# Performance work log

Hardware: AMD Instinct MI355X
Metric: run time of the kernel (lower is better)

Reference implementation:

```python
import jax, jax.numpy as jnp
import numpy as np

S, B, D, H = 1024, 8, 768, 12
PROMPT_NUM = 8
DH = D // H


def setup_inputs() -> dict:
    key = jax.random.key(0)
    ks = jax.random.split(key, 5)
    scale = 1.0 / np.sqrt(D)
    return {
        "x": jax.random.normal(ks[0], (S, B, D), dtype=jnp.float32),
        "in_proj_weight": jax.random.normal(ks[1], (3 * D, D), dtype=jnp.float32) * scale,
        "in_proj_bias": jax.random.normal(ks[2], (3 * D,), dtype=jnp.float32) * 0.02,
        "out_w": jax.random.normal(ks[3], (D, D), dtype=jnp.float32) * scale,
        "out_b": jax.random.normal(ks[4], (D,), dtype=jnp.float32) * 0.02,
    }


def reference(x, in_proj_weight, in_proj_bias, out_w, out_b):
    # x: (S, B, D) -> (B, S, D)
    xt = jnp.transpose(x, (1, 0, 2))
    qkv = xt @ in_proj_weight.T + in_proj_bias  # (B, S, 3D)
    q, k, v = jnp.split(qkv, 3, axis=-1)
    q = q.reshape(B, S, H, DH)
    k = k.reshape(B, S, H, DH)
    v = v.reshape(B, S, H, DH)
    # affinity (n, q, k, h); scale by sqrt(head_dim)
    aff = jnp.einsum("nqhc,nkhc->nqkh", q / np.sqrt(DH), k)
    # prompt masking: CLS_MASK | PROMPT_MASK
    tokens = S - PROMPT_NUM
    m = np.zeros((S, S), dtype=bool)
    m[0, tokens:] = True          # CLS_MASK: CLS query can't attend to prompts
    m[tokens:, tokens:] = True    # PROMPT_MASK: prompts can't attend to prompts
    m = jnp.asarray(m)
    aff = jnp.where(m[None, :, :, None], jnp.float32(-10000.0), aff)
    # softmax over key axis (dim=-2 of nqkh)
    aff = jax.nn.softmax(aff, axis=2)
    mix = jnp.einsum("nqlh,nlhc->nqhc", aff, v)  # (B, S, H, DH)
    out = mix.reshape(B, S, D) @ out_w.T + out_b
    # transpose back to (S, B, ...)
    return (
        jnp.transpose(q, (1, 0, 2, 3)),
        jnp.transpose(k, (1, 0, 2, 3)),
        jnp.transpose(v, (1, 0, 2, 3)),
        jnp.transpose(out, (1, 0, 2)),
    )
```

## Files before the change

kernel.cpp:

```cpp
#include <hip/hip_runtime.h>


typedef unsigned short u16;
typedef __attribute__((ext_vector_type(8))) short short8;
typedef __attribute__((ext_vector_type(4))) short short4v;
typedef __attribute__((ext_vector_type(4))) float floatx4;
typedef __attribute__((ext_vector_type(4))) unsigned short ushort4v;

#define NB 8
#define NS 1024
#define NH 12
#define ND 768
#define DHD 64
#define TOKENS 1016
#define QKV_OUT_STRIDE 6291456

#if __has_builtin(__builtin_amdgcn_exp2f)
#define EXP2(x) __builtin_amdgcn_exp2f(x)
#else
#define EXP2(x) exp2f(x)
#endif

#if defined(__HIP_DEVICE_COMPILE__)
  #if __has_builtin(__builtin_amdgcn_mfma_f32_16x16x16bf16_1k)
    #define MFMA16(a, b, c) __builtin_amdgcn_mfma_f32_16x16x16bf16_1k(a, b, c, 0, 0, 0)
  #else
    #define MFMA16(a, b, c) __builtin_amdgcn_mfma_f32_16x16x16_bf16(a, b, c, 0, 0, 0)
  #endif
  #define GLD16(g, l)                                                        \
    __builtin_amdgcn_global_load_lds(                                        \
        (const __attribute__((address_space(1))) void*)(g),                  \
        (__attribute__((address_space(3))) void*)(l), 16, 0, 0)
#else
  #define MFMA16(a, b, c) (c)
  #define GLD16(g, l) ((void)0)
#endif

__device__ __forceinline__ u16 f2bf(float f) {
  union { float f; unsigned u; } c; c.f = f;
  return (u16)((c.u + 0x7fffu + ((c.u >> 16) & 1u)) >> 16);
}

#define CVT_B0 6144
#define CVT_B1 1728
#define CVT_B2 576
__global__ __launch_bounds__(256) void cvt3(
    const float* __restrict__ s0, u16* __restrict__ d0,
    const float* __restrict__ s1, u16* __restrict__ d1,
    const float* __restrict__ s2, u16* __restrict__ d2) {
  int blk = blockIdx.x;
  const float* s; u16* d;
  if (blk < CVT_B0) { s = s0; d = d0; }
  else if (blk < CVT_B0 + CVT_B1) { s = s1; d = d1; blk -= CVT_B0; }
  else { s = s2; d = d2; blk -= CVT_B0 + CVT_B1; }
  const int i = (blk * 256 + (int)threadIdx.x) * 4;
  const float4 v = *(const float4*)(s + i);
  ushort4v o;
  o.x = f2bf(v.x); o.y = f2bf(v.y); o.z = f2bf(v.z); o.w = f2bf(v.w);
  *(ushort4v*)(d + i) = o;
}

__global__ __launch_bounds__(256) void qkv_gemm(
    const u16* __restrict__ Xb, const u16* __restrict__ Wb,
    const float* __restrict__ bias, float* __restrict__ out) {
  __shared__ __align__(16) u16 As[128][32];
  __shared__ __align__(16) u16 Bs[128][32];
  const int tid = threadIdx.x;
  const int lane = tid & 63, wave = tid >> 6;
  const int l15 = lane & 15, quad = lane >> 4;
  const int wm = wave & 1, wn = wave >> 1;
  const int mblk = blockIdx.x * 128;
  const int nblk = blockIdx.y * 128;

  floatx4 acc[4][4];
#pragma unroll
  for (int i = 0; i < 4; ++i)
#pragma unroll
    for (int j = 0; j < 4; ++j) acc[i][j] = (floatx4)0.f;

  const int lr = lane >> 2;
  const int lc = (lane & 3) * 8;
  const int c0 = wave * 2;
  const int r0 = c0 * 16 + lr, r1 = r0 + 16;
  const int gm0 = mblk + r0, gm1 = mblk + r1;
  const u16* ga0 = Xb + ((gm0 & 1023) * NB + (gm0 >> 10)) * ND + lc;
  const u16* ga1 = Xb + ((gm1 & 1023) * NB + (gm1 >> 10)) * ND + lc;
  const u16* gb0 = Wb + (nblk + r0) * ND + lc;
  const u16* gb1 = Wb + (nblk + r1) * ND + lc;
  u16* la0 = &As[c0 * 16][0];
  u16* la1 = &As[c0 * 16 + 16][0];
  u16* lb0 = &Bs[c0 * 16][0];
  u16* lb1 = &Bs[c0 * 16 + 16][0];

  for (int kt = 0; kt < 24; ++kt) {
    const int k0 = kt * 32;
    GLD16(ga0 + k0, la0);
    GLD16(ga1 + k0, la1);
    GLD16(gb0 + k0, lb0);
    GLD16(gb1 + k0, lb1);
    __syncthreads();
    short8 af[4], bfr[4];
#pragma unroll
    for (int mt = 0; mt < 4; ++mt)
      af[mt] = *(const short8*)&As[wm * 64 + mt * 16 + l15][quad * 8];
#pragma unroll
    for (int nt = 0; nt < 4; ++nt)
      bfr[nt] = *(const short8*)&Bs[wn * 64 + nt * 16 + l15][quad * 8];
#pragma unroll
    for (int mt = 0; mt < 4; ++mt)
#pragma unroll
      for (int nt = 0; nt < 4; ++nt)
        acc[mt][nt] = __builtin_amdgcn_mfma_f32_16x16x32_bf16(
            af[mt], bfr[nt], acc[mt][nt], 0, 0, 0);
    __syncthreads();
  }

#pragma unroll
  for (int mt = 0; mt < 4; ++mt) {
#pragma unroll
    for (int r = 0; r < 4; ++r) {
      const int gm = mblk + wm * 64 + mt * 16 + quad * 4 + r;
      const int b = gm >> 10, s = gm & 1023;
#pragma unroll
      for (int nt = 0; nt < 4; ++nt) {
        const int gn = nblk + wn * 64 + nt * 16 + l15;
        const int seg = gn / ND;
        const int nn = gn - seg * ND;
        out[seg * QKV_OUT_STRIDE + (s * NB + b) * ND + nn] = acc[mt][nt][r] + bias[gn];
      }
    }
  }
}

__global__ __launch_bounds__(256) void prep(
    const float* __restrict__ K, const float* __restrict__ V,
    u16* __restrict__ Kb, u16* __restrict__ Vt) {
  __shared__ u16 tile[DHD][40];
  const int t = threadIdx.x;
  const int bh = blockIdx.y;
  const int b = bh / NH, h = bh % NH;
  const int s0 = blockIdx.x * 32;
  const int sl = t >> 3;
  const int c0 = (t & 7) * 8;
  const int s = s0 + sl;
  if (blockIdx.z == 0) {
    const float* src = K + ((s * NB + b) * NH + h) * DHD + c0;
    const float4 v0 = *(const float4*)src;
    const float4 v1 = *(const float4*)(src + 4);
    short8 o;
    o[0] = f2bf(v0.x); o[1] = f2bf(v0.y); o[2] = f2bf(v0.z); o[3] = f2bf(v0.w);
    o[4] = f2bf(v1.x); o[5] = f2bf(v1.y); o[6] = f2bf(v1.z); o[7] = f2bf(v1.w);
    *(short8*)(Kb + ((size_t)bh * NS + s) * DHD + c0) = o;
  } else {
    const float* src = V + ((s * NB + b) * NH + h) * DHD + c0;
    const float4 v0 = *(const float4*)src;
    const float4 v1 = *(const float4*)(src + 4);
    tile[c0 + 0][sl] = f2bf(v0.x); tile[c0 + 1][sl] = f2bf(v0.y);
    tile[c0 + 2][sl] = f2bf(v0.z); tile[c0 + 3][sl] = f2bf(v0.w);
    tile[c0 + 4][sl] = f2bf(v1.x); tile[c0 + 5][sl] = f2bf(v1.y);
    tile[c0 + 6][sl] = f2bf(v1.z); tile[c0 + 7][sl] = f2bf(v1.w);
    __syncthreads();
    const int c = t >> 2;
    const int so = (t & 3) * 8;
    *(short8*)(Vt + ((size_t)bh * DHD + c) * NS + s0 + so) =
        *(const short8*)&tile[c][so];
  }
}

__global__ __launch_bounds__(256) void attn(
    const float* __restrict__ Q, const u16* __restrict__ Kb,
    const u16* __restrict__ Vt, u16* __restrict__ mix) {
  __shared__ __align__(16) u16 Kt[64][72];
  __shared__ __align__(16) u16 Vs[64][72];
  const int tid = threadIdx.x;
  const int lane = tid & 63, wave = tid >> 6;
  const int l15 = lane & 15, quad = lane >> 4;
  const int bh = blockIdx.y;
  const int b = bh / NH, h = bh % NH;
  const int qb = blockIdx.x * 128 + wave * 32;

  short8 qf[2][2];
  bool qmask[2];
#pragma unroll
  for (int j = 0; j < 2; ++j) {
    const int qj = qb + j * 16 + l15;
    qmask[j] = (qj == 0 || qj >= TOKENS);
    const float* qp = Q + ((qj * NB + b) * NH + h) * DHD + quad * 8;
#pragma unroll
    for (int e = 0; e < 8; ++e) {
      qf[j][0][e] = (short)f2bf(qp[e]);
      qf[j][1][e] = (short)f2bf(qp[32 + e]);
    }
  }

  floatx4 O[2][4];
#pragma unroll
  for (int j = 0; j < 2; ++j)
#pragma unroll
    for (int g = 0; g < 4; ++g) O[j][g] = (floatx4)0.f;
  float li[2] = {0.f, 0.f};

  const u16* kg = Kb + (size_t)bh * NS * DHD;
  const u16* vg = Vt + (size_t)bh * DHD * NS;

  const float C1 = 0.125f * 1.44269504089f;
  const float C0 = -10.0f * 1.44269504089f;

  const int srow = tid >> 2;
  const int scol = (tid & 3) * 16;

  short8 pk0, pk1, pv0, pv1;
  {
    pk0 = *(const short8*)(kg + srow * DHD + scol);
    pk1 = *(const short8*)(kg + srow * DHD + scol + 8);
    pv0 = *(const short8*)(vg + srow * NS + scol);
    pv1 = *(const short8*)(vg + srow * NS + scol + 8);
  }

  for (int it = 0; it < 16; ++it) {
    *(short8*)&Kt[srow][scol] = pk0;
    *(short8*)&Kt[srow][scol + 8] = pk1;
    *(short8*)&Vs[srow][scol] = pv0;
    *(short8*)&Vs[srow][scol + 8] = pv1;
    __syncthreads();
    if (it < 15) {
      const int k0 = (it + 1) * 64;
      pk0 = *(const short8*)(kg + (k0 + srow) * DHD + scol);
      pk1 = *(const short8*)(kg + (k0 + srow) * DHD + scol + 8);
      pv0 = *(const short8*)(vg + srow * NS + k0 + scol);
      pv1 = *(const short8*)(vg + srow * NS + k0 + scol + 8);
    }
    const bool mrow = (it == 15) && (quad >= 2);
#pragma unroll
    for (int sub = 0; sub < 4; ++sub) {
      const short8 kf0 = *(const short8*)&Kt[sub * 16 + l15][quad * 8];
      const short8 kf1 = *(const short8*)&Kt[sub * 16 + l15][32 + quad * 8];
      short4v pb[2];
#pragma unroll
      for (int j = 0; j < 2; ++j) {
        floatx4 a = (floatx4)0.f;
        a = __builtin_amdgcn_mfma_f32_16x16x32_bf16(kf0, qf[j][0], a, 0, 0, 0);
        a = __builtin_amdgcn_mfma_f32_16x16x32_bf16(kf1, qf[j][1], a, 0, 0, 0);
        float p[4];
#pragma unroll
        for (int r = 0; r < 4; ++r) p[r] = EXP2(fmaf(a[r], C1, C0));
        if (sub == 3 && mrow && qmask[j]) {
#pragma unroll
          for (int r = 0; r < 4; ++r) p[r] = 0.f;
        }
        li[j] += (p[0] + p[1]) + (p[2] + p[3]);
#pragma unroll
        for (int r = 0; r < 4; ++r) pb[j][r] = (short)f2bf(p[r]);
      }
#pragma unroll
      for (int g = 0; g < 4; ++g) {
        const short4v vf = *(const short4v*)&Vs[g * 16 + l15][sub * 16 + quad * 4];
        O[0][g] = MFMA16(vf, pb[0], O[0][g]);
        O[1][g] = MFMA16(vf, pb[1], O[1][g]);
      }
    }
    __syncthreads();
  }

#pragma unroll
  for (int j = 0; j < 2; ++j) {
    float l = li[j];
    l += __shfl_xor(l, 16);
    l += __shfl_xor(l, 32);
    const float rl = 1.0f / l;
    const int qj = qb + j * 16 + l15;
    u16* mp = mix + ((size_t)b * NS + qj) * ND + h * DHD + quad * 4;
#pragma unroll
    for (int g = 0; g < 4; ++g) {
      ushort4v o;
#pragma unroll
      for (int r = 0; r < 4; ++r) o[r] = f2bf(O[j][g][r] * rl);
      *(ushort4v*)(mp + g * 16) = o;
    }
  }
}

__global__ __launch_bounds__(256) void out_gemm(
    const u16* __restrict__ A, const u16* __restrict__ Wb,
    const float* __restrict__ bias, float* __restrict__ out) {
  __shared__ __align__(16) u16 As[128][32];
  __shared__ __align__(16) u16 Bs[128][32];
  const int tid = threadIdx.x;
  const int lane = tid & 63, wave = tid >> 6;
  const int l15 = lane & 15, quad = lane >> 4;
  const int wm = wave & 1, wn = wave >> 1;
  const int mblk = blockIdx.x * 128;
  const int nblk = blockIdx.y * 128;

  floatx4 acc[4][4];
#pragma unroll
  for (int i = 0; i < 4; ++i)
#pragma unroll
    for (int j = 0; j < 4; ++j) acc[i][j] = (floatx4)0.f;

  const int lr = lane >> 2;
  const int lc = (lane & 3) * 8;
  const int c0 = wave * 2;
  const int r0 = c0 * 16 + lr, r1 = r0 + 16;
  const u16* ga0 = A + (mblk + r0) * ND + lc;
  const u16* ga1 = A + (mblk + r1) * ND + lc;
  const u16* gb0 = Wb + (nblk + r0) * ND + lc;
  const u16* gb1 = Wb + (nblk + r1) * ND + lc;
  u16* la0 = &As[c0 * 16][0];
  u16* la1 = &As[c0 * 16 + 16][0];
  u16* lb0 = &Bs[c0 * 16][0];
  u16* lb1 = &Bs[c0 * 16 + 16][0];

  for (int kt = 0; kt < 24; ++kt) {
    const int k0 = kt * 32;
    GLD16(ga0 + k0, la0);
    GLD16(ga1 + k0, la1);
    GLD16(gb0 + k0, lb0);
    GLD16(gb1 + k0, lb1);
    __syncthreads();
    short8 af[4], bfr[4];
#pragma unroll
    for (int mt = 0; mt < 4; ++mt)
      af[mt] = *(const short8*)&As[wm * 64 + mt * 16 + l15][quad * 8];
#pragma unroll
    for (int nt = 0; nt < 4; ++nt)
      bfr[nt] = *(const short8*)&Bs[wn * 64 + nt * 16 + l15][quad * 8];
#pragma unroll
    for (int mt = 0; mt < 4; ++mt)
#pragma unroll
      for (int nt = 0; nt < 4; ++nt)
        acc[mt][nt] = __builtin_amdgcn_mfma_f32_16x16x32_bf16(
            af[mt], bfr[nt], acc[mt][nt], 0, 0, 0);
    __syncthreads();
  }

#pragma unroll
  for (int mt = 0; mt < 4; ++mt) {
#pragma unroll
    for (int r = 0; r < 4; ++r) {
      const int gm = mblk + wm * 64 + mt * 16 + quad * 4 + r;
      const int b = gm >> 10, s = gm & 1023;
#pragma unroll
      for (int nt = 0; nt < 4; ++nt) {
        const int gn = nblk + wn * 64 + nt * 16 + l15;
        out[(s * NB + b) * ND + gn] = acc[mt][nt][r] + bias[gn];
      }
    }
  }
}

extern "C" void kernel_launch(void* const* d_in, const int* in_sizes, int n_in,
                              void* d_out, int out_size, void* d_ws, size_t ws_size,
                              hipStream_t stream) {
  const float* X  = (const float*)d_in[0];
  const float* W  = (const float*)d_in[1];
  const float* Bi = (const float*)d_in[2];
  const float* Ow = (const float*)d_in[3];
  const float* Ob = (const float*)d_in[4];
  float* out = (float*)d_out;

  u16* Xb  = (u16*)d_ws;
  u16* Wb  = Xb  + 6291456;
  u16* Owb = Wb  + 1769472;
  u16* Vt  = Owb + 589824;
  u16* Kb  = Vt  + 6291456;
  u16* mix = Kb  + 6291456;

  cvt3<<<CVT_B0 + CVT_B1 + CVT_B2, 256, 0, stream>>>(X, Xb, W, Wb, Ow, Owb);
  qkv_gemm<<<dim3(64, 18), 256, 0, stream>>>(Xb, Wb, Bi, out);
  prep<<<dim3(32, 96, 2), 256, 0, stream>>>(out + QKV_OUT_STRIDE,
                                            out + 2 * QKV_OUT_STRIDE, Kb, Vt);
  attn<<<dim3(8, 96), 256, 0, stream>>>(out, Kb, Vt, mix);
  out_gemm<<<dim3(64, 6), 256, 0, stream>>>(mix, Owb, Ob, out + 3 * QKV_OUT_STRIDE);
}
```

Baseline: 244.7 us.

## Double-buffer GEMM LDS tiles, remap attention blocks across XCDs, pack bf16 conversion

Both GEMM kernels now use two LDS buffers, so the global-to-LDS load of the next K tile is issued while MFMAs run on the current one. This is meant to hide global load latency, at the cost of twice the shared memory per block. The attention kernel remaps the linear block id so that all query blocks of the same batch-head land on the same XCD, aiming for better L2 reuse of K and V. It also converts the probabilities to bf16 with a packed two-element intrinsic instead of per-element conversion.

```diff
diff --git a/kernel.cpp b/kernel.cpp
--- a/kernel.cpp
+++ b/kernel.cpp
@@ -1,4 +1,5 @@
 #include <hip/hip_runtime.h>
+#include <hip/hip_bf16.h>
 
 
 typedef unsigned short u16;
@@ -6,6 +7,7 @@
 typedef __attribute__((ext_vector_type(4))) short short4v;
 typedef __attribute__((ext_vector_type(4))) float floatx4;
 typedef __attribute__((ext_vector_type(4))) unsigned short ushort4v;
+typedef __attribute__((ext_vector_type(2))) unsigned int uint2v;
 
 #define NB 8
 #define NS 1024
@@ -60,11 +62,38 @@
   *(ushort4v*)(d + i) = o;
 }
 
+#define GEMM_STAGE(buf, k0)                                                  \
+  do {                                                                       \
+    GLD16(ga0 + (k0), &buf##A[c0 * 16][0]);                                  \
+    GLD16(ga1 + (k0), &buf##A[c0 * 16 + 16][0]);                             \
+    GLD16(gb0 + (k0), &buf##B[c0 * 16][0]);                                  \
+    GLD16(gb1 + (k0), &buf##B[c0 * 16 + 16][0]);                             \
+  } while (0)
+
+#define GEMM_COMPUTE(buf)                                                    \
+  do {                                                                       \
+    short8 af[4], bfr[4];                                                    \
+    _Pragma("unroll")                                                        \
+    for (int mt = 0; mt < 4; ++mt)                                           \
+      af[mt] = *(const short8*)&buf##A[wm * 64 + mt * 16 + l15][quad * 8];   \
+    _Pragma("unroll")                                                        \
+    for (int nt = 0; nt < 4; ++nt)                                           \
+      bfr[nt] = *(const short8*)&buf##B[wn * 64 + nt * 16 + l15][quad * 8];  \
+    _Pragma("unroll")                                                        \
+    for (int mt = 0; mt < 4; ++mt)                                           \
+      _Pragma("unroll")                                                      \
+      for (int nt = 0; nt < 4; ++nt)                                         \
+        acc[mt][nt] = __builtin_amdgcn_mfma_f32_16x16x32_bf16(               \
+            af[mt], bfr[nt], acc[mt][nt], 0, 0, 0);                          \
+  } while (0)
+
 __global__ __launch_bounds__(256) void qkv_gemm(
     const u16* __restrict__ Xb, const u16* __restrict__ Wb,
     const float* __restrict__ bias, float* __restrict__ out) {
-  __shared__ __align__(16) u16 As[128][32];
-  __shared__ __align__(16) u16 Bs[128][32];
+  __shared__ __align__(16) u16 p0A[128][32];
+  __shared__ __align__(16) u16 p0B[128][32];
+  __shared__ __align__(16) u16 p1A[128][32];
+  __shared__ __align__(16) u16 p1B[128][32];
   const int tid = threadIdx.x;
   const int lane = tid & 63, wave = tid >> 6;
   const int l15 = lane & 15, quad = lane >> 4;
@@ -87,31 +116,15 @@
   const u16* ga1 = Xb + ((gm1 & 1023) * NB + (gm1 >> 10)) * ND + lc;
   const u16* gb0 = Wb + (nblk + r0) * ND + lc;
   const u16* gb1 = Wb + (nblk + r1) * ND + lc;
-  u16* la0 = &As[c0 * 16][0];
-  u16* la1 = &As[c0 * 16 + 16][0];
-  u16* lb0 = &Bs[c0 * 16][0];
-  u16* lb1 = &Bs[c0 * 16 + 16][0];
-
-  for (int kt = 0; kt < 24; ++kt) {
-    const int k0 = kt * 32;
-    GLD16(ga0 + k0, la0);
-    GLD16(ga1 + k0, la1);
-    GLD16(gb0 + k0, lb0);
-    GLD16(gb1 + k0, lb1);
-    __syncthreads();
-    short8 af[4], bfr[4];
-#pragma unroll
-    for (int mt = 0; mt < 4; ++mt)
-      af[mt] = *(const short8*)&As[wm * 64 + mt * 16 + l15][quad * 8];
-#pragma unroll
-    for (int nt = 0; nt < 4; ++nt)
-      bfr[nt] = *(const short8*)&Bs[wn * 64 + nt * 16 + l15][quad * 8];
-#pragma unroll
-    for (int mt = 0; mt < 4; ++mt)
-#pragma unroll
-      for (int nt = 0; nt < 4; ++nt)
-        acc[mt][nt] = __builtin_amdgcn_mfma_f32_16x16x32_bf16(
-            af[mt], bfr[nt], acc[mt][nt], 0, 0, 0);
+
+  GEMM_STAGE(p0, 0);
+  __syncthreads();
+  for (int kt = 0; kt < 24; kt += 2) {
+    GEMM_STAGE(p1, (kt + 1) * 32);
+    GEMM_COMPUTE(p0);
+    __syncthreads();
+    if (kt + 2 < 24) GEMM_STAGE(p0, (kt + 2) * 32);
+    GEMM_COMPUTE(p1);
     __syncthreads();
   }
 
@@ -175,9 +188,12 @@
   const int tid = threadIdx.x;
   const int lane = tid & 63, wave = tid >> 6;
   const int l15 = lane & 15, quad = lane >> 4;
-  const int bh = blockIdx.y;
+  const int L = (int)blockIdx.x + 8 * (int)blockIdx.y;
+  const int xcd = L & 7, tt = L >> 3;
+  const int bh = xcd + 8 * (tt >> 3);
+  const int qx = tt & 7;
   const int b = bh / NH, h = bh % NH;
-  const int qb = blockIdx.x * 128 + wave * 32;
+  const int qb = qx * 128 + wave * 32;
 
   short8 qf[2][2];
   bool qmask[2];
@@ -249,8 +265,12 @@
           for (int r = 0; r < 4; ++r) p[r] = 0.f;
         }
         li[j] += (p[0] + p[1]) + (p[2] + p[3]);
-#pragma unroll
-        for (int r = 0; r < 4; ++r) pb[j][r] = (short)f2bf(p[r]);
+        __hip_bfloat162 w0 = __float22bfloat162_rn(make_float2(p[0], p[1]));
+        __hip_bfloat162 w1 = __float22bfloat162_rn(make_float2(p[2], p[3]));
+        uint2v pw;
+        pw.x = *(const unsigned*)&w0;
+        pw.y = *(const unsigned*)&w1;
+        pb[j] = __builtin_bit_cast(short4v, pw);
       }
 #pragma unroll
       for (int g = 0; g < 4; ++g) {
@@ -283,8 +303,10 @@
 __global__ __launch_bounds__(256) void out_gemm(
     const u16* __restrict__ A, const u16* __restrict__ Wb,
     const float* __restrict__ bias, float* __restrict__ out) {
-  __shared__ __align__(16) u16 As[128][32];
-  __shared__ __align__(16) u16 Bs[128][32];
+  __shared__ __align__(16) u16 p0A[128][32];
+  __shared__ __align__(16) u16 p0B[128][32];
+  __shared__ __align__(16) u16 p1A[128][32];
+  __shared__ __align__(16) u16 p1B[128][32];
   const int tid = threadIdx.x;
   const int lane = tid & 63, wave = tid >> 6;
   const int l15 = lane & 15, quad = lane >> 4;
@@ -306,31 +328,15 @@
   const u16* ga1 = A + (mblk + r1) * ND + lc;
   const u16* gb0 = Wb + (nblk + r0) * ND + lc;
   const u16* gb1 = Wb + (nblk + r1) * ND + lc;
-  u16* la0 = &As[c0 * 16][0];
-  u16* la1 = &As[c0 * 16 + 16][0];
-  u16* lb0 = &Bs[c0 * 16][0];
-  u16* lb1 = &Bs[c0 * 16 + 16][0];
-
-  for (int kt = 0; kt < 24; ++kt) {
-    const int k0 = kt * 32;
-    GLD16(ga0 + k0, la0);
-    GLD16(ga1 + k0, la1);
-    GLD16(gb0 + k0, lb0);
-    GLD16(gb1 + k0, lb1);
-    __syncthreads();
-    short8 af[4], bfr[4];
-#pragma unroll
-    for (int mt = 0; mt < 4; ++mt)
-      af[mt] = *(const short8*)&As[wm * 64 + mt * 16 + l15][quad * 8];
-#pragma unroll
-    for (int nt = 0; nt < 4; ++nt)
-      bfr[nt] = *(const short8*)&Bs[wn * 64 + nt * 16 + l15][quad * 8];
-#pragma unroll
-    for (int mt = 0; mt < 4; ++mt)
-#pragma unroll
-      for (int nt = 0; nt < 4; ++nt)
-        acc[mt][nt] = __builtin_amdgcn_mfma_f32_16x16x32_bf16(
-            af[mt], bfr[nt], acc[mt][nt], 0, 0, 0);
+
+  GEMM_STAGE(p0, 0);
+  __syncthreads();
+  for (int kt = 0; kt < 24; kt += 2) {
+    GEMM_STAGE(p1, (kt + 1) * 32);
+    GEMM_COMPUTE(p0);
+    __syncthreads();
+    if (kt + 2 < 24) GEMM_STAGE(p0, (kt + 2) * 32);
+    GEMM_COMPUTE(p1);
     __syncthreads();
   }
 
```

After: 246.7 us. About the same (+0.8%).
